# Kernel tuning notes

Measured on AMD Instinct MI355X. Metric: run time of the kernel, lower is better.

## Reference

```python
import jax, jax.numpy as jnp
import numpy as np

N = 100000   # nodes
E = 3200000  # edges
M = 4096     # moves
K = 16       # orders per move
NEG_SLOPE = 0.2  # PyG GATv2Conv default negative_slope

PARAM_SHAPES = {
    'g1_Wl': (10, 15), 'g1_Wr': (10, 15), 'g1_att': (10,), 'g1_b': (10,),
    'g2_Wl': (10, 25), 'g2_Wr': (10, 25), 'g2_att': (10,), 'g2_b': (10,),
    'g3_Wl': (10, 25), 'g3_Wr': (10, 25), 'g3_att': (10,), 'g3_b': (10,),
    'vt_W': (20, 29), 'vt_b': (20,), 'va_W': (1, 20), 'va_b': (1,),
    'vv_W': (10, 20), 'vv_b': (10,), 'vl_W': (1, 10), 'vl_b': (1,),
    'at_W': (20, 48), 'at_b': (20,), 'dt_W': (20, 23), 'dt_b': (20,),
    'oa_W': (1, 20), 'oa_b': (1,), 'ov_W': (1, 20), 'ov_b': (1,),
}
PARAM_NAMES = list(PARAM_SHAPES.keys())


def _linear(x, W, b):
    return x @ W.T + b


def _gatv2(x, src, dst, Wl, Wr, att, b):
    # GATv2Conv (heads=1, self-loops appended by caller), eval mode (no dropout)
    xl = x @ Wl.T  # messages from source nodes
    xr = x @ Wr.T
    e = (jax.nn.leaky_relu(xl[src] + xr[dst], NEG_SLOPE) * att).sum(-1)  # [E+N]
    emax = jax.ops.segment_max(e, dst, num_segments=N)
    ee = jnp.exp(e - emax[dst])
    denom = jax.ops.segment_sum(ee, dst, num_segments=N)
    alpha = ee / denom[dst]
    return jax.ops.segment_sum(alpha[:, None] * xl[src], dst, num_segments=N) + b


def _forward(x1, x2, edges, move_src, move_dst, move_armies, is_attack, params):
    (g1_Wl, g1_Wr, g1_att, g1_b,
     g2_Wl, g2_Wr, g2_att, g2_b,
     g3_Wl, g3_Wr, g3_att, g3_b,
     vt_W, vt_b, va_W, va_b, vv_W, vv_b, vl_W, vl_b,
     at_W, at_b, dt_W, dt_b, oa_W, oa_b, ov_W, ov_b) = params
    x2t = jnp.tile(x2, (N, 1))  # [N,4]
    self_idx = jnp.arange(N, dtype=edges.dtype)
    src = jnp.concatenate([edges[0], self_idx])
    dst = jnp.concatenate([edges[1], self_idx])
    x = jax.nn.relu(_gatv2(x1, src, dst, g1_Wl, g1_Wr, g1_att, g1_b))
    x = jax.nn.relu(_gatv2(jnp.concatenate([x, x1], 1), src, dst, g2_Wl, g2_Wr, g2_att, g2_b))
    x = jax.nn.relu(_gatv2(jnp.concatenate([x, x1], 1), src, dst, g3_Wl, g3_Wr, g3_att, g3_b))  # [N,10]
    # per-move order tensors (vectorized over [M,K]); deploy uses move_src as target
    xs, xd = x[move_src], x[move_dst]       # [M,K,10]
    x1s, x1d = x1[move_src], x1[move_dst]   # [M,K,15]
    extra = 0.6 * move_armies - 0.7 * (x1d[..., 3] + x1d[..., 4])
    attack_in = jnp.concatenate([xs, xd, x1s[..., 3:], x1d[..., 1:],
                                 move_armies[..., None], extra[..., None]], -1)  # [M,K,48]
    deploy_in = jnp.concatenate([xs, x1s[..., 3:], move_armies[..., None]], -1)  # [M,K,23]
    feat = jnp.where(is_attack[..., None] == 1,
                     _linear(attack_in, at_W, at_b),
                     _linear(deploy_in, dt_W, dt_b))
    feat = jax.nn.relu(feat)  # dropout = identity (eval)
    attn = jax.nn.softmax(_linear(feat, oa_W, oa_b), axis=1)  # softmax over orders
    p = (attn * _linear(feat, ov_W, ov_b)).sum(axis=(1, 2))   # [M]
    # value head: attention pooling over all nodes
    Vn = jax.nn.relu(_linear(jnp.concatenate([x, x1, x2t], 1), vt_W, vt_b))  # [N,20]
    vatt = jax.nn.softmax(_linear(Vn, va_W, va_b), axis=0)
    Vp = jax.nn.relu((vatt * _linear(Vn, vv_W, vv_b)).sum(axis=0))
    V = jnp.tanh(_linear(Vp, vl_W, vl_b))[0]
    return V, jax.nn.log_softmax(p, axis=0)


def setup_inputs() -> dict:
    key = jax.random.key(0)
    ks = iter(jax.random.split(key, 64))
    inp = {
        'x1': jax.random.normal(next(ks), (N, 15), jnp.float32),
        'x2': jax.random.normal(next(ks), (4,), jnp.float32),
        'edges': jax.random.randint(next(ks), (2, E), 0, N, jnp.int32),
        'move_src': jax.random.randint(next(ks), (M, K), 0, N, jnp.int32),
        'move_dst': jax.random.randint(next(ks), (M, K), 0, N, jnp.int32),
        'move_armies': jax.random.uniform(next(ks), (M, K), jnp.float32) * 10.0,
        'is_attack': jax.random.randint(next(ks), (M, K), 0, 2, jnp.int32),
    }
    for name, shape in PARAM_SHAPES.items():
        inp[name] = jax.random.normal(next(ks), shape, jnp.float32) * 0.1
    return inp


def reference(x1, x2, edges, move_src, move_dst, move_armies, is_attack,
              g1_Wl, g1_Wr, g1_att, g1_b, g2_Wl, g2_Wr, g2_att, g2_b,
              g3_Wl, g3_Wr, g3_att, g3_b, vt_W, vt_b, va_W, va_b,
              vv_W, vv_b, vl_W, vl_b, at_W, at_b, dt_W, dt_b,
              oa_W, oa_b, ov_W, ov_b):
    params = (g1_Wl, g1_Wr, g1_att, g1_b, g2_Wl, g2_Wr, g2_att, g2_b,
              g3_Wl, g3_Wr, g3_att, g3_b, vt_W, vt_b, va_W, va_b,
              vv_W, vv_b, vl_W, vl_b, at_W, at_b, dt_W, dt_b,
              oa_W, oa_b, ov_W, ov_b)
    return _forward(x1, x2, edges, move_src, move_dst, move_armies, is_attack, params)
```

## Files before the change

### kernel.cpp

```cpp
#include <hip/hip_runtime.h>
#include <hip/hip_fp16.h>
#include <math.h>

#define NN 100000
#define NE 3200000
#define MM 4096
#define KK 16
#define NEG_SLOPE 0.2f
#define SUB 8
#define BSH 8
#define NB 391
#define PCH 8192
#define FCAP 12288
#define XS 12
#define XSU 4
#define PART_BLOCKS ((NE + NN + PCH - 1) / PCH)
#define LIN_BLOCKS  ((NN + 511) / 512)
#define MOVE_BLOCKS ((MM * KK) / 256)
#define VAL_BLOCKS  ((NN + 255) / 256)
#define CSTR 16
#define SENT 0xFFFFFFFFu
#define PZ ((int)0xAAAAAAAAu)

typedef float vfloat2 __attribute__((__vector_size__(2 * sizeof(float))));

__device__ __forceinline__ void f8x10_decode(const uint4& w, float* xs) {
    vfloat2 f0 = __builtin_amdgcn_cvt_pk_f32_fp8(w.x, false); xs[0]=f0[0]; xs[1]=f0[1];
    vfloat2 f1 = __builtin_amdgcn_cvt_pk_f32_fp8(w.x, true);  xs[2]=f1[0]; xs[3]=f1[1];
    vfloat2 f2 = __builtin_amdgcn_cvt_pk_f32_fp8(w.y, false); xs[4]=f2[0]; xs[5]=f2[1];
    vfloat2 f3 = __builtin_amdgcn_cvt_pk_f32_fp8(w.y, true);  xs[6]=f3[0]; xs[7]=f3[1];
    vfloat2 f4 = __builtin_amdgcn_cvt_pk_f32_fp8(w.z, false); xs[8]=f4[0]; xs[9]=f4[1];
}
__device__ __forceinline__ uint4 f8x10_encode(const float* v) {
    unsigned u0 = __builtin_amdgcn_cvt_pk_fp8_f32(v[0], v[1], 0, false);
    u0 = __builtin_amdgcn_cvt_pk_fp8_f32(v[2], v[3], u0, true);
    unsigned u1 = __builtin_amdgcn_cvt_pk_fp8_f32(v[4], v[5], 0, false);
    u1 = __builtin_amdgcn_cvt_pk_fp8_f32(v[6], v[7], u1, true);
    unsigned u2 = __builtin_amdgcn_cvt_pk_fp8_f32(v[8], v[9], 0, false);
    return make_uint4(u0, u1, u2, 0u);
}

__device__ __forceinline__ void load_x1_row(const float* __restrict__ x1, int node, float* r) {
    const float* p = x1 + (long)node * 15;
    float4 a = *(const float4*)(p);
    float4 b = *(const float4*)(p + 4);
    float4 c = *(const float4*)(p + 8);
    float4 d = *(const float4*)(p + 11);
    r[0]=a.x; r[1]=a.y; r[2]=a.z; r[3]=a.w;
    r[4]=b.x; r[5]=b.y; r[6]=b.z; r[7]=b.w;
    r[8]=c.x; r[9]=c.y; r[10]=c.z; r[11]=d.x;
    r[12]=d.y; r[13]=d.z; r[14]=d.w;
}

__global__ __launch_bounds__(512) void part_lin1_kernel(const int* __restrict__ edges,
                                                        int* __restrict__ cnt,
                                                        unsigned* __restrict__ recs,
                                                        const float* __restrict__ x1,
                                                        const float* __restrict__ Wl,
                                                        const float* __restrict__ Wr,
                                                        unsigned* __restrict__ xl8,
                                                        float* __restrict__ xr) {
    int t = threadIdx.x;
    if (blockIdx.x >= PART_BLOCKS) {
        int i = (blockIdx.x - PART_BLOCKS) * 512 + t;
        if (i >= NN) return;
        float in[15];
        #pragma unroll
        for (int j = 0; j < 15; j++) in[j] = x1[(long)i * 15 + j];
        float sl[10];
        #pragma unroll
        for (int o = 0; o < 10; o++) {
            float l = 0.f, r = 0.f;
            #pragma unroll
            for (int j = 0; j < 15; j++) {
                l += Wl[o * 15 + j] * in[j];
                r += Wr[o * 15 + j] * in[j];
            }
            sl[o] = l;
            xr[(long)i * XS + o] = r;
        }
        *(uint4*)(xl8 + (long)i * XSU) = f8x10_encode(sl);
        return;
    }
    __shared__ unsigned srt[PCH];
    __shared__ unsigned short sbk[PCH];
    __shared__ int scn[512];
    __shared__ int h[NB];
    __shared__ int gb[NB];
    __shared__ int cur[NB];
    __shared__ int lb[NB];
    const int total = NE + NN;
    int base = blockIdx.x * PCH;
    int n = min(PCH, total - base);
    for (int b = t; b < NB; b += 512) { h[b] = 0; cur[b] = 0; }
    __syncthreads();
    for (int j = t; j < n; j += 512) {
        int i = base + j;
        int d = (i < NE) ? edges[NE + i] : (i - NE);
        atomicAdd(&h[d >> BSH], 1);
    }
    __syncthreads();
    for (int b = t; b < NB; b += 512) {
        int hv = h[b];
        if (hv > 0) {
            int padded = (hv + 15) & ~15;
            gb[b] = atomicAdd(&cnt[b * CSTR], padded) - PZ;
            atomicAdd(&cnt[b * CSTR + 1], hv);
        }
    }
    scn[t] = (t < NB) ? h[t] : 0;
    __syncthreads();
    for (int off = 1; off < 512; off <<= 1) {
        int v = (t >= off) ? scn[t - off] : 0;
        __syncthreads();
        scn[t] += v;
        __syncthreads();
    }
    if (t < NB) lb[t] = scn[t] - h[t];
    __syncthreads();
    for (int j = t; j < n; j += 512) {
        int i = base + j;
        int s, d;
        if (i < NE) { s = edges[i]; d = edges[NE + i]; }
        else        { s = i - NE; d = s; }
        int b = d >> BSH;
        int slot = lb[b] + atomicAdd(&cur[b], 1);
        srt[slot] = ((unsigned)(d & 255) << 17) | (unsigned)s;
        sbk[slot] = (unsigned short)b;
    }
    __syncthreads();
    for (int j = t; j < n; j += 512) {
        int b = sbk[j];
        int gpos = gb[b] + (j - lb[b]);
        if (gpos >= 0 && gpos < FCAP) recs[(long)b * FCAP + gpos] = srt[j];
    }
    for (int b = t; b < NB; b += 512) {
        int hv = h[b];
        if (hv > 0) {
            int padded = (hv + 15) & ~15;
            for (int q = hv; q < padded; q++) {
                int gpos = gb[b] + q;
                if (gpos >= 0 && gpos < FCAP) recs[(long)b * FCAP + gpos] = SENT;
            }
        }
    }
}

__global__ __launch_bounds__(1024) void fine_sort_kernel(const unsigned* __restrict__ recs,
                                                         const int* __restrict__ cnt,
                                                         int* __restrict__ csr_src,
                                                         int* __restrict__ offsets) {
    __shared__ unsigned srt2[FCAP];
    __shared__ int scn[512];
    __shared__ int hist[256];
    __shared__ int sc[256];
    __shared__ int hb[257];
    __shared__ int cur[256];
    int b = blockIdx.x;
    int t = threadIdx.x;
    if (t < 512) {
        int c = (t < NB) ? min(max(cnt[t * CSTR + 1] - PZ, 0), FCAP) : 0;
        scn[t] = c;
    }
    __syncthreads();
    for (int off = 1; off < 512; off <<= 1) {
        int v = 0;
        if (t < 512 && t >= off) v = scn[t - off];
        __syncthreads();
        if (t < 512) scn[t] += v;
        __syncthreads();
    }
    int beg = (b == 0) ? 0 : scn[b - 1];
    int nbp = min(max(cnt[b * CSTR] - PZ, 0), FCAP);
    int nbr = min(max(cnt[b * CSTR + 1] - PZ, 0), FCAP);
    int nodebase = b << BSH;
    int nnodes = min(256, NN - nodebase);
    if (t < 256) { hist[t] = 0; cur[t] = 0; }
    __syncthreads();
    const unsigned* rsrc = recs + (long)b * FCAP;
    for (int j = t; j < nbp; j += 1024) {
        unsigned r = rsrc[j];
        if (r != SENT) atomicAdd(&hist[r >> 17], 1);
    }
    __syncthreads();
    int hv = (t < 256) ? hist[t] : 0;
    if (t < 256) sc[t] = hv;
    __syncthreads();
    for (int off = 1; off < 256; off <<= 1) {
        int v = 0;
        if (t < 256 && t >= off) v = sc[t - off];
        __syncthreads();
        if (t < 256) sc[t] += v;
        __syncthreads();
    }
    if (t < 256) hb[t] = sc[t] - hv;
    if (t == 0) hb[256] = nbr;
    __syncthreads();
    for (int j = t; j < nbp; j += 1024) {
        unsigned r = rsrc[j];
        if (r != SENT) {
            int l = r >> 17;
            int p = hb[l] + atomicAdd(&cur[l], 1);
            srt2[p] = r & 0x1FFFFu;
        }
    }
    __syncthreads();
    for (int j = t; j < nbr; j += 1024)
        csr_src[beg + j] = (int)srt2[j];
    if (t < nnodes) offsets[nodebase + t] = beg + hb[t];
    if (b == NB - 1 && t == 0) offsets[NN] = beg + nbr;
}

template<bool FUSE_NEXT>
__global__ void gat_aggregate_kernel(const int* __restrict__ csr_src,
                                     const int* __restrict__ offsets,
                                     const unsigned* __restrict__ xl8,
                                     const float* __restrict__ xr,
                                     const float* __restrict__ att,
                                     const float* __restrict__ b,
                                     const float* __restrict__ x1,
                                     const float* __restrict__ nWl,
                                     const float* __restrict__ nWr,
                                     unsigned* __restrict__ xlo,
                                     float* __restrict__ xro,
                                     float* __restrict__ xout)
{
    int t = blockIdx.x * blockDim.x + threadIdx.x;
    int node = t / SUB;
    int lane = t % SUB;
    if (node >= NN) return;
    float xrn[12], a[10];
    const float4* xr4 = (const float4*)(xr + (long)node * XS);
    #pragma unroll
    for (int q = 0; q < 3; q++) {
        float4 v = xr4[q];
        xrn[4*q] = v.x; xrn[4*q+1] = v.y; xrn[4*q+2] = v.z; xrn[4*q+3] = v.w;
    }
    #pragma unroll
    for (int h = 0; h < 10; h++) a[h] = att[h];
    int beg = offsets[node], end = offsets[node + 1];
    float den = 0.f, num[10];
    #pragma unroll
    for (int h = 0; h < 10; h++) num[h] = 0.f;
    for (int jb = beg + lane; jb < end; jb += 8 * SUB) {
        int ss[8];
        bool vv[8];
        #pragma unroll
        for (int q = 0; q < 8; q++) {
            int jk = jb + q * SUB;
            vv[q] = (jk < end);
            ss[q] = csr_src[vv[q] ? jk : beg];
        }
        uint4 wa[8];
        #pragma unroll
        for (int q = 0; q < 8; q++)
            wa[q] = *(const uint4*)(xl8 + (long)ss[q] * XSU);
        #pragma unroll
        for (int q = 0; q < 8; q++) {
            float xs[10];
            f8x10_decode(wa[q], xs);
            float e = 0.f;
            #pragma unroll
            for (int h = 0; h < 10; h++) {
                float v = xs[h] + xrn[h];
                v = (v >= 0.f) ? v : NEG_SLOPE * v;
                e += v * a[h];
            }
            float w = vv[q] ? __expf(e) : 0.f;
            den += w;
            #pragma unroll
            for (int h = 0; h < 10; h++) num[h] += w * xs[h];
        }
    }
    #pragma unroll
    for (int off = SUB / 2; off; off >>= 1) {
        den += __shfl_xor(den, off, SUB);
        #pragma unroll
        for (int h = 0; h < 10; h++) num[h] += __shfl_xor(num[h], off, SUB);
    }
    float inv = 1.f / den;
    float xo[10];
    #pragma unroll
    for (int h = 0; h < 10; h++) xo[h] = fmaxf(num[h] * inv + b[h], 0.f);
    if (FUSE_NEXT) {
        if (lane < 5) {
            float in2[25];
            #pragma unroll
            for (int h = 0; h < 10; h++) in2[h] = xo[h];
            #pragma unroll
            for (int h = 0; h < 15; h++) in2[10 + h] = x1[(long)node * 15 + h];
            int o0 = 2 * lane, o1 = 2 * lane + 1;
            float sl0 = 0.f, sl1 = 0.f, sr0 = 0.f, sr1 = 0.f;
            #pragma unroll
            for (int jj = 0; jj < 25; jj++) {
                sl0 += nWl[o0 * 25 + jj] * in2[jj];
                sl1 += nWl[o1 * 25 + jj] * in2[jj];
                sr0 += nWr[o0 * 25 + jj] * in2[jj];
                sr1 += nWr[o1 * 25 + jj] * in2[jj];
            }
            unsigned pk = __builtin_amdgcn_cvt_pk_fp8_f32(sl0, sl1, 0, false);
            ((unsigned short*)(xlo + (long)node * XSU))[lane] = (unsigned short)pk;
            *(float2*)(xro + (long)node * XS + o0) = make_float2(sr0, sr1);
        }
    } else {
        if (lane == 0) {
            #pragma unroll
            for (int h = 0; h < 10; h++) xout[(long)node * XS + h] = xo[h];
        }
    }
}

__global__ void move_value_kernel(const float* __restrict__ x,
                                  const float* __restrict__ x1,
                                  const float* __restrict__ x2,
                                  const int* __restrict__ msrc,
                                  const int* __restrict__ mdst,
                                  const float* __restrict__ armies,
                                  const int* __restrict__ isatk,
                                  const float* __restrict__ at_W, const float* __restrict__ at_b,
                                  const float* __restrict__ dt_W, const float* __restrict__ dt_b,
                                  const float* __restrict__ oa_W, const float* __restrict__ oa_b,
                                  const float* __restrict__ ov_W, const float* __restrict__ ov_b,
                                  const float* __restrict__ vt_W, const float* __restrict__ vt_b,
                                  const float* __restrict__ va_W, const float* __restrict__ va_b,
                                  const float* __restrict__ vv_W, const float* __restrict__ vv_b,
                                  float* __restrict__ p,
                                  float* __restrict__ partials) {
    if (blockIdx.x < MOVE_BLOCKS) {
        int t = blockIdx.x * 256 + threadIdx.x;
        int m = t >> 4;
        int k = t & 15;
        int s = msrc[t], d = mdst[t];
        float arm = armies[t];
        bool atk = (isatk[t] == 1);
        float xsrc[12];
        const float4* xs4 = (const float4*)(x + (long)s * XS);
        #pragma unroll
        for (int q = 0; q < 3; q++) {
            float4 v = xs4[q];
            xsrc[4*q]=v.x; xsrc[4*q+1]=v.y; xsrc[4*q+2]=v.z; xsrc[4*q+3]=v.w;
        }
        float x1s[15];
        load_x1_row(x1, s, x1s);
        float feat[20];
        if (atk) {
            float in[48];
            #pragma unroll
            for (int h = 0; h < 10; h++) in[h] = xsrc[h];
            const float4* xd4 = (const float4*)(x + (long)d * XS);
            float xdst[12];
            #pragma unroll
            for (int q = 0; q < 3; q++) {
                float4 v = xd4[q];
                xdst[4*q]=v.x; xdst[4*q+1]=v.y; xdst[4*q+2]=v.z; xdst[4*q+3]=v.w;
            }
            float x1d[15];
            load_x1_row(x1, d, x1d);
            #pragma unroll
            for (int h = 0; h < 10; h++) in[10 + h] = xdst[h];
            #pragma unroll
            for (int h = 0; h < 12; h++) in[20 + h] = x1s[3 + h];
            #pragma unroll
            for (int h = 0; h < 14; h++) in[32 + h] = x1d[1 + h];
            in[46] = arm;
            in[47] = 0.6f * arm - 0.7f * (x1d[3] + x1d[4]);
            #pragma unroll
            for (int o = 0; o < 20; o++) {
                float sum = at_b[o];
                #pragma unroll
                for (int j = 0; j < 48; j++) sum += at_W[o * 48 + j] * in[j];
                feat[o] = fmaxf(sum, 0.f);
            }
        } else {
            float in[23];
            #pragma unroll
            for (int h = 0; h < 10; h++) in[h] = xsrc[h];
            #pragma unroll
            for (int h = 0; h < 12; h++) in[10 + h] = x1s[3 + h];
            in[22] = arm;
            #pragma unroll
            for (int o = 0; o < 20; o++) {
                float sum = dt_b[o];
                #pragma unroll
                for (int j = 0; j < 23; j++) sum += dt_W[o * 23 + j] * in[j];
                feat[o] = fmaxf(sum, 0.f);
            }
        }
        float oa = oa_b[0], ov = ov_b[0];
        #pragma unroll
        for (int j = 0; j < 20; j++) {
            oa += oa_W[j] * feat[j];
            ov += ov_W[j] * feat[j];
        }
        float mx = oa;
        #pragma unroll
        for (int off = 8; off; off >>= 1) mx = fmaxf(mx, __shfl_xor(mx, off, 16));
        float w = __expf(oa - mx);
        float nume = w * ov;
        float den = w;
        #pragma unroll
        for (int off = 8; off; off >>= 1) {
            nume += __shfl_xor(nume, off, 16);
            den  += __shfl_xor(den,  off, 16);
        }
        if (k == 0) p[m] = nume / den;
        return;
    }
    __shared__ float sm[4][11];
    int vb = blockIdx.x - MOVE_BLOCKS;
    int i = vb * 256 + threadIdx.x;
    float w = 0.f;
    float acc[10];
    #pragma unroll
    for (int h = 0; h < 10; h++) acc[h] = 0.f;
    if (i < NN) {
        float in[29];
        const float4* xi4 = (const float4*)(x + (long)i * XS);
        float xi[12];
        #pragma unroll
        for (int q = 0; q < 3; q++) {
            float4 v = xi4[q];
            xi[4*q]=v.x; xi[4*q+1]=v.y; xi[4*q+2]=v.z; xi[4*q+3]=v.w;
        }
        #pragma unroll
        for (int h = 0; h < 10; h++) in[h] = xi[h];
        float x1r[15];
        load_x1_row(x1, i, x1r);
        #pragma unroll
        for (int h = 0; h < 15; h++) in[10 + h] = x1r[h];
        float4 x2v = *(const float4*)x2;
        in[25] = x2v.x; in[26] = x2v.y; in[27] = x2v.z; in[28] = x2v.w;
        float Vn[20];
        #pragma unroll
        for (int o = 0; o < 20; o++) {
            float s = vt_b[o];
            #pragma unroll
            for (int j = 0; j < 29; j++) s += vt_W[o * 29 + j] * in[j];
            Vn[o] = fmaxf(s, 0.f);
        }
        float lg = va_b[0];
        #pragma unroll
        for (int j = 0; j < 20; j++) lg += va_W[j] * Vn[j];
        w = __expf(lg);
        #pragma unroll
        for (int o = 0; o < 10; o++) {
            float s = vv_b[o];
            #pragma unroll
            for (int j = 0; j < 20; j++) s += vv_W[o * 20 + j] * Vn[j];
            acc[o] = w * s;
        }
    }
    #pragma unroll
    for (int off = 32; off; off >>= 1) {
        w += __shfl_xor(w, off, 64);
        #pragma unroll
        for (int h = 0; h < 10; h++) acc[h] += __shfl_xor(acc[h], off, 64);
    }
    int wid = threadIdx.x >> 6;
    if ((threadIdx.x & 63) == 0) {
        #pragma unroll
        for (int h = 0; h < 10; h++) sm[wid][h] = acc[h];
        sm[wid][10] = w;
    }
    __syncthreads();
    if (threadIdx.x < 11) {
        int c = threadIdx.x;
        partials[(long)vb * 12 + c] = sm[0][c] + sm[1][c] + sm[2][c] + sm[3][c];
    }
}

__global__ void final_kernel(const float* __restrict__ p,
                             const float* __restrict__ partials,
                             const float* __restrict__ vl_W, const float* __restrict__ vl_b,
                             float* __restrict__ out) {
    if (blockIdx.x == 0) {
        __shared__ float sm[256];
        int tid = threadIdx.x;
        float mx = -INFINITY;
        for (int i = tid; i < MM; i += 256) mx = fmaxf(mx, p[i]);
        sm[tid] = mx; __syncthreads();
        for (int s = 128; s; s >>= 1) { if (tid < s) sm[tid] = fmaxf(sm[tid], sm[tid + s]); __syncthreads(); }
        mx = sm[0]; __syncthreads();
        float sum = 0.f;
        for (int i = tid; i < MM; i += 256) sum += expf(p[i] - mx);
        sm[tid] = sum; __syncthreads();
        for (int s = 128; s; s >>= 1) { if (tid < s) sm[tid] += sm[tid + s]; __syncthreads(); }
        float ls = mx + logf(sm[0]);
        for (int i = tid; i < MM; i += 256) out[1 + i] = p[i] - ls;
    } else if (threadIdx.x < 64) {
        int lane = threadIdx.x;
        float s[11];
        #pragma unroll
        for (int c = 0; c < 11; c++) s[c] = 0.f;
        for (int j = lane; j < VAL_BLOCKS; j += 64)
            #pragma unroll
            for (int c = 0; c < 11; c++) s[c] += partials[(long)j * 12 + c];
        #pragma unroll
        for (int off = 32; off; off >>= 1)
            #pragma unroll
            for (int c = 0; c < 11; c++) s[c] += __shfl_xor(s[c], off, 64);
        if (lane == 0) {
            float inv = 1.0f / s[10];
            float v = vl_b[0];
            #pragma unroll
            for (int h = 0; h < 10; h++) v += vl_W[h] * fmaxf(s[h] * inv, 0.f);
            out[0] = tanhf(v);
        }
    }
}

extern "C" void kernel_launch(void* const* d_in, const int* in_sizes, int n_in,
                              void* d_out, int out_size, void* d_ws, size_t ws_size,
                              hipStream_t stream) {
    const float* x1      = (const float*)d_in[0];
    const float* x2      = (const float*)d_in[1];
    const int*   edges   = (const int*)d_in[2];
    const int*   msrc    = (const int*)d_in[3];
    const int*   mdst    = (const int*)d_in[4];
    const float* armies  = (const float*)d_in[5];
    const int*   isatk   = (const int*)d_in[6];
    const float* g1_Wl = (const float*)d_in[7],  *g1_Wr = (const float*)d_in[8];
    const float* g1_att= (const float*)d_in[9],  *g1_b  = (const float*)d_in[10];
    const float* g2_Wl = (const float*)d_in[11], *g2_Wr = (const float*)d_in[12];
    const float* g2_att= (const float*)d_in[13], *g2_b  = (const float*)d_in[14];
    const float* g3_Wl = (const float*)d_in[15], *g3_Wr = (const float*)d_in[16];
    const float* g3_att= (const float*)d_in[17], *g3_b  = (const float*)d_in[18];
    const float* vt_W  = (const float*)d_in[19], *vt_b  = (const float*)d_in[20];
    const float* va_W  = (const float*)d_in[21], *va_b  = (const float*)d_in[22];
    const float* vv_W  = (const float*)d_in[23], *vv_b  = (const float*)d_in[24];
    const float* vl_W  = (const float*)d_in[25], *vl_b  = (const float*)d_in[26];
    const float* at_W  = (const float*)d_in[27], *at_b  = (const float*)d_in[28];
    const float* dt_W  = (const float*)d_in[29], *dt_b  = (const float*)d_in[30];
    const float* oa_W  = (const float*)d_in[31], *oa_b  = (const float*)d_in[32];
    const float* ov_W  = (const float*)d_in[33], *ov_b  = (const float*)d_in[34];

    float* out = (float*)d_out;

    float* ws = (float*)d_ws;
    unsigned* xl8A = (unsigned*)ws;
    unsigned* xl8B = xl8A + (long)NN * XSU;
    float* xrA = (float*)(xl8B + (long)NN * XSU);
    float* xrB = xrA + (long)NN * XS;
    float* xF  = xrB + (long)NN * XS;
    int* csr_src = (int*)(xF + (long)NN * XS);
    int* offsets = csr_src + (NE + NN);
    unsigned* recs = (unsigned*)(offsets + NN + 16);
    int* cnt   = (int*)(recs + (long)NB * FCAP);
    float* pbuf = (float*)(cnt + NB * CSTR + 16);
    float* partials = pbuf + MM;

    const int aggBlocks = ((long)NN * SUB + 255) / 256;

    part_lin1_kernel<<<PART_BLOCKS + LIN_BLOCKS, 512, 0, stream>>>(
        edges, cnt, recs, x1, g1_Wl, g1_Wr, xl8A, xrA);
    fine_sort_kernel<<<NB, 1024, 0, stream>>>(recs, cnt, csr_src, offsets);
    gat_aggregate_kernel<true><<<aggBlocks, 256, 0, stream>>>(
        csr_src, offsets, xl8A, xrA, g1_att, g1_b, x1, g2_Wl, g2_Wr, xl8B, xrB, nullptr);
    gat_aggregate_kernel<true><<<aggBlocks, 256, 0, stream>>>(
        csr_src, offsets, xl8B, xrB, g2_att, g2_b, x1, g3_Wl, g3_Wr, xl8A, xrA, nullptr);
    gat_aggregate_kernel<false><<<aggBlocks, 256, 0, stream>>>(
        csr_src, offsets, xl8A, xrA, g3_att, g3_b, x1, nullptr, nullptr, nullptr, nullptr, xF);
    move_value_kernel<<<MOVE_BLOCKS + VAL_BLOCKS, 256, 0, stream>>>(
        xF, x1, x2, msrc, mdst, armies, isatk,
        at_W, at_b, dt_W, dt_b, oa_W, oa_b, ov_W, ov_b,
        vt_W, vt_b, va_W, va_b, vv_W, vv_b, pbuf, partials);
    final_kernel<<<2, 256, 0, stream>>>(pbuf, partials, vl_W, vl_b, out);
}
```

Baseline: 317.4 us.

## Fuse first GAT aggregation into fine sort kernel using shared-memory CSR

The first GATv2 layer's aggregation (plus the layer-2 linear projection) now runs inside the fine-sort kernel. It reads each bucket's sorted source indices straight from shared memory instead of writing the CSR and launching a separate aggregation pass. This removes one kernel launch and the global reload of csr_src and offsets for layer 1. In exchange, the sort kernel gains register pressure and its per-block work grows, with only 391 blocks of 1024 threads each handling 256 nodes, which may limit parallelism for the aggregation phase.

Result: no change. 321.6 us (+1.3%).

```diff
diff --git a/kernel.cpp b/kernel.cpp
--- a/kernel.cpp
+++ b/kernel.cpp
@@ -146,10 +146,21 @@
     }
 }
 
-__global__ __launch_bounds__(1024) void fine_sort_kernel(const unsigned* __restrict__ recs,
-                                                         const int* __restrict__ cnt,
-                                                         int* __restrict__ csr_src,
-                                                         int* __restrict__ offsets) {
+__global__ __launch_bounds__(1024) void fine_sort_agg1_kernel(
+        const unsigned* __restrict__ recs,
+        const int* __restrict__ cnt,
+        int* __restrict__ csr_src,
+        int* __restrict__ offsets,
+        const unsigned* __restrict__ xl8,
+        const float* __restrict__ xr,
+        const float* __restrict__ att,
+        const float* __restrict__ bias,
+        const float* __restrict__ x1,
+        const float* __restrict__ nWl,
+        const float* __restrict__ nWr,
+        unsigned* __restrict__ xlo,
+        float* __restrict__ xro)
+{
     __shared__ unsigned srt2[FCAP];
     __shared__ int scn[512];
     __shared__ int hist[256];
@@ -209,6 +220,89 @@
         csr_src[beg + j] = (int)srt2[j];
     if (t < nnodes) offsets[nodebase + t] = beg + hb[t];
     if (b == NB - 1 && t == 0) offsets[NN] = beg + nbr;
+    int lane = t & 7;
+    int vloc = t >> 3;
+    float a[10];
+    #pragma unroll
+    for (int h = 0; h < 10; h++) a[h] = att[h];
+    for (int half = 0; half < 2; half++) {
+        int v = vloc + half * 128;
+        if (v < nnodes) {
+            int node = nodebase + v;
+            int ebeg = hb[v], eend = hb[v + 1];
+            float xrn[10];
+            {
+                const float4* xr4 = (const float4*)(xr + (long)node * XS);
+                float4 r0 = xr4[0], r1 = xr4[1];
+                float2 r2 = *(const float2*)(xr + (long)node * XS + 8);
+                xrn[0]=r0.x; xrn[1]=r0.y; xrn[2]=r0.z; xrn[3]=r0.w;
+                xrn[4]=r1.x; xrn[5]=r1.y; xrn[6]=r1.z; xrn[7]=r1.w;
+                xrn[8]=r2.x; xrn[9]=r2.y;
+            }
+            float den = 0.f, num[10];
+            #pragma unroll
+            for (int h = 0; h < 10; h++) num[h] = 0.f;
+            for (int jb = ebeg + lane; jb < eend; jb += 4 * 8) {
+                int ss[4];
+                bool vvq[4];
+                #pragma unroll
+                for (int q = 0; q < 4; q++) {
+                    int jk = jb + q * 8;
+                    vvq[q] = (jk < eend);
+                    ss[q] = (int)srt2[vvq[q] ? jk : ebeg];
+                }
+                uint4 wa[4];
+                #pragma unroll
+                for (int q = 0; q < 4; q++)
+                    wa[q] = *(const uint4*)(xl8 + (long)ss[q] * XSU);
+                #pragma unroll
+                for (int q = 0; q < 4; q++) {
+                    float xs[10];
+                    f8x10_decode(wa[q], xs);
+                    float e = 0.f;
+                    #pragma unroll
+                    for (int h = 0; h < 10; h++) {
+                        float vv2 = xs[h] + xrn[h];
+                        vv2 = (vv2 >= 0.f) ? vv2 : NEG_SLOPE * vv2;
+                        e += vv2 * a[h];
+                    }
+                    float w = vvq[q] ? __expf(e) : 0.f;
+                    den += w;
+                    #pragma unroll
+                    for (int h = 0; h < 10; h++) num[h] += w * xs[h];
+                }
+            }
+            #pragma unroll
+            for (int off = 4; off; off >>= 1) {
+                den += __shfl_xor(den, off, 8);
+                #pragma unroll
+                for (int h = 0; h < 10; h++) num[h] += __shfl_xor(num[h], off, 8);
+            }
+            float inv = 1.f / den;
+            float xo[10];
+            #pragma unroll
+            for (int h = 0; h < 10; h++) xo[h] = fmaxf(num[h] * inv + bias[h], 0.f);
+            if (lane < 5) {
+                float in2[25];
+                #pragma unroll
+                for (int h = 0; h < 10; h++) in2[h] = xo[h];
+                #pragma unroll
+                for (int h = 0; h < 15; h++) in2[10 + h] = x1[(long)node * 15 + h];
+                int o0 = 2 * lane, o1 = 2 * lane + 1;
+                float sl0 = 0.f, sl1 = 0.f, sr0 = 0.f, sr1 = 0.f;
+                #pragma unroll
+                for (int jj = 0; jj < 25; jj++) {
+                    sl0 += nWl[o0 * 25 + jj] * in2[jj];
+                    sl1 += nWl[o1 * 25 + jj] * in2[jj];
+                    sr0 += nWr[o0 * 25 + jj] * in2[jj];
+                    sr1 += nWr[o1 * 25 + jj] * in2[jj];
+                }
+                unsigned pk = __builtin_amdgcn_cvt_pk_fp8_f32(sl0, sl1, 0, false);
+                ((unsigned short*)(xlo + (long)node * XSU))[lane] = (unsigned short)pk;
+                *(float2*)(xro + (long)node * XS + o0) = make_float2(sr0, sr1);
+            }
+        }
+    }
 }
 
 template<bool FUSE_NEXT>
@@ -553,9 +647,9 @@
 
     part_lin1_kernel<<<PART_BLOCKS + LIN_BLOCKS, 512, 0, stream>>>(
         edges, cnt, recs, x1, g1_Wl, g1_Wr, xl8A, xrA);
-    fine_sort_kernel<<<NB, 1024, 0, stream>>>(recs, cnt, csr_src, offsets);
-    gat_aggregate_kernel<true><<<aggBlocks, 256, 0, stream>>>(
-        csr_src, offsets, xl8A, xrA, g1_att, g1_b, x1, g2_Wl, g2_Wr, xl8B, xrB, nullptr);
+    fine_sort_agg1_kernel<<<NB, 1024, 0, stream>>>(
+        recs, cnt, csr_src, offsets, xl8A, xrA, g1_att, g1_b,
+        x1, g2_Wl, g2_Wr, xl8B, xrB);
     gat_aggregate_kernel<true><<<aggBlocks, 256, 0, stream>>>(
         csr_src, offsets, xl8B, xrB, g2_att, g2_b, x1, g3_Wl, g3_Wr, xl8A, xrA, nullptr);
     gat_aggregate_kernel<false><<<aggBlocks, 256, 0, stream>>>(
```
